# Optimization experiments

Measured on AMD Instinct MI355X. Metric: run time of the kernel, lower is better.

## Reference

```python
import jax, jax.numpy as jnp
import numpy as np

K_SIZE, STRIDE, PAD = 3, 1, 1
B, C1, C2, H, W = 2, 256, 256, 64, 64


def conv2d(x, w, b, stride, pad):
    out = jax.lax.conv_general_dilated(
        x, w, (stride, stride), [(pad, pad), (pad, pad)],
        dimension_numbers=("NCHW", "OIHW", "NCHW"))
    return out + b[None, :, None, None]


def deform_conv2d(x, offset, mask, w, b, k, stride, pad):
    # torchvision.ops.deform_conv2d semantics (modulated, offset_groups=1)
    Bn, C, Hh, Ww = x.shape
    Ho, Wo = offset.shape[2], offset.shape[3]
    K = k * k
    # offset channels are (dy, dx) interleaved per kernel point
    off = offset.reshape(Bn, K, 2, Ho, Wo)
    dy, dx = off[:, :, 0], off[:, :, 1]          # [B,K,Ho,Wo]
    ki = jnp.arange(k)
    kyy, kxx = jnp.meshgrid(ki, ki, indexing="ij")
    kyy, kxx = kyy.reshape(K), kxx.reshape(K)
    base_y = (jnp.arange(Ho) * stride - pad)[None, :, None] + kyy[:, None, None]  # [K,Ho,1]
    base_x = (jnp.arange(Wo) * stride - pad)[None, None, :] + kxx[:, None, None]  # [K,1,Wo]
    ys = base_y[None].astype(x.dtype) + dy       # [B,K,Ho,Wo]
    xs = base_x[None].astype(x.dtype) + dx
    N = K * Ho * Wo
    ysf, xsf = ys.reshape(Bn, N), xs.reshape(Bn, N)
    y0 = jnp.floor(ysf)
    x0 = jnp.floor(xsf)
    ly, lx = ysf - y0, xsf - x0                  # bilinear fractions
    y0i, x0i = y0.astype(jnp.int32), x0.astype(jnp.int32)
    xf = x.reshape(Bn, C, Hh * Ww)

    def gather(yi, xi):
        valid = (yi >= 0) & (yi < Hh) & (xi >= 0) & (xi < Ww)
        idx = jnp.clip(yi, 0, Hh - 1) * Ww + jnp.clip(xi, 0, Ww - 1)
        v = jnp.take_along_axis(xf, idx[:, None, :], axis=2)  # [B,C,N]
        return v * valid[:, None, :].astype(x.dtype)

    v00 = gather(y0i, x0i)
    v01 = gather(y0i, x0i + 1)
    v10 = gather(y0i + 1, x0i)
    v11 = gather(y0i + 1, x0i + 1)
    wy1, wx1 = ly[:, None], lx[:, None]
    val = (v00 * (1 - wy1) * (1 - wx1) + v01 * (1 - wy1) * wx1 +
           v10 * wy1 * (1 - wx1) + v11 * wy1 * wx1)          # [B,C,N]
    val = val.reshape(Bn, C, K, Ho, Wo) * mask[:, None]       # modulate
    out = jnp.einsum("ock,bckhw->bohw", w.reshape(w.shape[0], C, K), val)
    return out + b[None, :, None, None]


def setup_inputs() -> dict:
    key = jax.random.key(0)
    ks = jax.random.split(key, 6)
    k2 = K_SIZE * K_SIZE
    return {
        "x": jax.random.normal(ks[0], (B, C1, H, W), jnp.float32),
        "offset_feat": jax.random.normal(ks[1], (B, C2, H, W), jnp.float32),
        # offset/mask head conv (zero-init in module; small random so offsets are non-trivial)
        "w_offset_mask": jax.random.normal(ks[2], (3 * k2, C2, K_SIZE, K_SIZE), jnp.float32) * 0.01,
        "b_offset_mask": jax.random.normal(ks[3], (3 * k2,), jnp.float32) * 0.01,
        "w_dcn": jax.random.normal(ks[4], (C2, C1, K_SIZE, K_SIZE), jnp.float32) / np.sqrt(C1 * k2),
        "b_dcn": jax.random.normal(ks[5], (C2,), jnp.float32) * 0.01,
    }


def reference(x, offset_feat, w_offset_mask, b_offset_mask, w_dcn, b_dcn):
    om = conv2d(offset_feat, w_offset_mask, b_offset_mask, STRIDE, PAD)  # [B,3*k*k,Ho,Wo]
    o1, o2, m = jnp.split(om, 3, axis=1)
    offset = jnp.concatenate([o1, o2], axis=1)   # [B,2*k*k,Ho,Wo]
    mask = jax.nn.sigmoid(m)                      # [B,k*k,Ho,Wo]
    return deform_conv2d(x, offset, mask, w_dcn, b_dcn, K_SIZE, STRIDE, PAD)
```

## Files before the change

### kernel.cpp

```cpp
#include <hip/hip_runtime.h>
#include <math.h>

#define BATCH 2
#define CIN   256
#define COUT  256
#define COFF  256
#define HWPIX 4096
#define CKTOT 2304
#define VSTR  40
#define PH    66
#define PHW   4356
#define NKG   12

typedef __attribute__((ext_vector_type(8))) short short8;
typedef __attribute__((ext_vector_type(8))) unsigned short ushort8;
typedef __attribute__((ext_vector_type(4))) float float4v;

__device__ __forceinline__ unsigned short f2bf(float f) {
    unsigned u = __float_as_uint(f);
    unsigned r = (u + 0x7FFFu + ((u >> 16) & 1u)) >> 16;
    return (unsigned short)r;
}
__device__ __forceinline__ float bf2f(unsigned short h) {
    return __uint_as_float(((unsigned)h) << 16);
}

__global__ __launch_bounds__(256) void prep_kernel(
    const float* __restrict__ x, const float* __restrict__ feat,
    const float* __restrict__ wdcn, const float* __restrict__ wom,
    unsigned short* __restrict__ xTh,
    unsigned short* __restrict__ fh,
    unsigned short* __restrict__ whi,
    unsigned short* __restrict__ wohi,
    float* __restrict__ out)
{
    const int bid = blockIdx.x;
    const int tid = threadIdx.x;

    if (bid < 4096) {
        const bool isx = bid < 2048;
        const int lb = isx ? bid : bid - 2048;
        const int b  = lb >> 10;
        const int r  = lb & 1023;
        const int pt = r >> 3;
        const int ct = r & 7;
        __shared__ float t[32][33];
        const int tx = tid & 31, ty = tid >> 5;
        const float* src = isx ? x : feat;
        const float* sb = src + ((size_t)b * 256 + ct * 32) * HWPIX + pt * 32;
#pragma unroll
        for (int i = ty; i < 32; i += 8)
            t[i][tx] = sb[(size_t)i * HWPIX + tx];
        __syncthreads();
        if (isx) {
            unsigned short* ob = xTh + ((size_t)b * HWPIX + pt * 32) * 256 + ct * 32;
#pragma unroll
            for (int i = ty; i < 32; i += 8)
                ob[(size_t)i * 256 + tx] = f2bf(t[tx][i]);
        } else {
#pragma unroll
            for (int i = ty; i < 32; i += 8) {
                int p = pt * 32 + i;
                int row = (p >> 6) + 1, col = (p & 63) + 1;
                fh[((size_t)b * PHW + row * PH + col) * 256 + ct * 32 + tx]
                    = f2bf(t[tx][i]);
            }
        }
    } else if (bid < 6400) {
        int gid = (bid - 4096) * 256 + tid;
        int cc  = gid & 31;
        int co  = (gid >> 5) & 255;
        int kcb = gid >> 13;
        int k   = kcb >> 3;
        int cb  = kcb & 7;
        float w = wdcn[((size_t)co * 256 + cb * 32 + cc) * 9 + k];
        whi[gid] = f2bf(w);
    } else if (bid < 6688) {
        int gid = (bid - 6400) * 256 + tid;
        int cc  = gid & 31;
        int co  = (gid >> 5) & 31;
        int kcb = gid >> 10;
        int k   = kcb >> 3;
        int cb  = kcb & 7;
        float w = 0.0f;
        if (co < 27) w = wom[(size_t)co * CKTOT + (cb * 32 + cc) * 9 + k];
        wohi[gid] = f2bf(w);
    } else if (bid < 7208) {
        int idx = (bid - 6688) * 256 + tid;
        int b = idx / 66560;
        int r = idx - b * 66560;
        int pidx = r >> 8;
        int c = r & 255;
        int row, col;
        if (pidx < 66)       { row = 0;           col = pidx; }
        else if (pidx < 132) { row = 65;          col = pidx - 66; }
        else if (pidx < 196) { row = pidx - 131;  col = 0; }
        else                 { row = pidx - 195;  col = 65; }
        fh[((size_t)b * PHW + row * PH + col) * 256 + c] = 0;
    } else {
        int idx = (bid - 7208) * 256 + tid;
        ((float4*)out)[idx] = make_float4(0.f, 0.f, 0.f, 0.f);
    }
}

__global__ __launch_bounds__(256) void conv_om_mfma_kernel(
    const unsigned short* __restrict__ fh,
    const unsigned short* __restrict__ wohi,
    float* __restrict__ om12)
{
    const int y  = blockIdx.x;
    const int kg = blockIdx.y;
    const int b  = blockIdx.z;
    const int tid = threadIdx.x;
    const int wv  = tid >> 6;
    const int lane = tid & 63;
    const int l15 = lane & 15;
    const int q   = lane >> 4;
    const int xg  = wv * 16 + l15;

    float4v acc[2];
    acc[0] = (float4v)0.0f;
    acc[1] = (float4v)0.0f;

    const unsigned short* fhb = fh + (size_t)b * PHW * 256;

#pragma unroll 3
    for (int i = 0; i < 6; ++i) {
        int kcb = kg * 6 + i;
        int k  = kcb >> 3;
        int cb = kcb & 7;
        size_t s = ((size_t)((y + k / 3) * PH + xg + k % 3)) * 256 + cb * 32 + q * 8;
        short8 bh = *(const short8*)(fhb + s);
        short8 ah0 = *(const short8*)(wohi + ((size_t)kcb * 32 + l15) * 32 + q * 8);
        short8 ah1 = *(const short8*)(wohi + ((size_t)kcb * 32 + 16 + l15) * 32 + q * 8);
        acc[0] = __builtin_amdgcn_mfma_f32_16x16x32_bf16(ah0, bh, acc[0], 0, 0, 0);
        acc[1] = __builtin_amdgcn_mfma_f32_16x16x32_bf16(ah1, bh, acc[1], 0, 0, 0);
    }

    const int p = y * 64 + xg;
    float* ob = om12 + (size_t)(kg * 2 + b) * 27 * HWPIX;
#pragma unroll
    for (int t = 0; t < 2; ++t) {
#pragma unroll
        for (int r = 0; r < 4; ++r) {
            int co = t * 16 + q * 4 + r;
            if (co < 27) ob[co * HWPIX + p] = acc[t][r];
        }
    }
}

__global__ __launch_bounds__(256) void finalize_om_kernel(
    const float* __restrict__ om12,
    const float* __restrict__ bom,
    float4* __restrict__ wt4,
    int4*   __restrict__ ix4)
{
    const int gid = blockIdx.x * 256 + threadIdx.x;
    const int p  = gid & 4095;
    const int bk = gid >> 12;
    const int b  = bk / 9;
    const int k  = bk - b * 9;

    float dy = bom[2 * k], dx = bom[2 * k + 1], mm = bom[18 + k];
#pragma unroll
    for (int g = 0; g < NKG; ++g) {
        const float* ob = om12 + (size_t)(g * 2 + b) * 27 * HWPIX;
        dy += ob[(2 * k) * HWPIX + p];
        dx += ob[(2 * k + 1) * HWPIX + p];
        mm += ob[(18 + k) * HWPIX + p];
    }
    const int yy = p >> 6, xx = p & 63;
    float ys = (float)(yy - 1 + (k / 3)) + dy;
    float xs = (float)(xx - 1 + (k % 3)) + dx;
    float y0f = floorf(ys), x0f = floorf(xs);
    int y0 = (int)y0f, x0 = (int)x0f;
    float ly = ys - y0f, lx = xs - x0f;
    float m  = 1.0f / (1.0f + expf(-mm));
    bool yv0 = ((unsigned)y0 < 64u), yv1 = ((unsigned)(y0 + 1) < 64u);
    bool xv0 = ((unsigned)x0 < 64u), xv1 = ((unsigned)(x0 + 1) < 64u);
    int i00 = (y0 * 64 + x0) << 8;
    float4 wt;
    int4 ix;
    wt.x = (yv0 && xv0) ? (1.0f - ly) * (1.0f - lx) * m : 0.0f;
    wt.y = (yv0 && xv1) ? (1.0f - ly) * lx * m          : 0.0f;
    wt.z = (yv1 && xv0) ? ly * (1.0f - lx) * m          : 0.0f;
    wt.w = (yv1 && xv1) ? ly * lx * m                   : 0.0f;
    ix.x = (yv0 && xv0) ? i00          : 0;
    ix.y = (yv0 && xv1) ? i00 + 256    : 0;
    ix.z = (yv1 && xv0) ? i00 + 16384  : 0;
    ix.w = (yv1 && xv1) ? i00 + 16640  : 0;
    wt4[gid] = wt;
    ix4[gid] = ix;
}

__global__ __launch_bounds__(512, 4) void dcn_mfma_kernel(
    const unsigned short* __restrict__ xTh,
    const float4* __restrict__ wt4,
    const int4* __restrict__ ix4,
    const unsigned short* __restrict__ whi,
    const float* __restrict__ bdcn,
    float* __restrict__ out)
{
    const int tid = threadIdx.x;
    const int y   = blockIdx.x >> 1;
    const int xh  = blockIdx.x & 1;
    const int kg  = blockIdx.y;
    const int b   = blockIdx.z;

    __shared__ float4 s_wt[288];
    __shared__ int4   s_ix[288];
    __shared__ unsigned short V[288 * VSTR];

    if (tid < 288) {
        int k   = tid >> 5;
        int pxl = tid & 31;
        int p   = y * 64 + xh * 32 + pxl;
        int src = ((b * 9 + k) << 12) + p;
        s_wt[tid] = wt4[src];
        s_ix[tid] = ix4[src];
    }
    __syncthreads();

    const int w    = tid >> 6;
    const int lane = tid & 63;
    const int l15  = lane & 15;
    const int q    = lane >> 4;

    const int cg   = tid & 3;
    const int spx  = (tid >> 2) & 31;
    const int tapg = tid >> 7;

    float4v acc[2][2];
#pragma unroll
    for (int t = 0; t < 2; ++t)
#pragma unroll
        for (int p = 0; p < 2; ++p) acc[t][p] = (float4v)0.0f;

    const unsigned short* xb = xTh + ((size_t)b << 12) * 256;

    for (int cbl = 0; cbl < 4; ++cbl) {
        const int cb = kg * 4 + cbl;

        {
            const unsigned short* xc = xb + cb * 32 + cg * 8;
#pragma unroll 3
            for (int j = 0; j < 3; ++j) {
                int k = tapg + 4 * j;
                if (k > 8) break;
                int cidx = k * 32 + spx;
                float4 wt = s_wt[cidx];
                int4   ix = s_ix[cidx];
                ushort8 u00 = *(const ushort8*)(xc + ix.x);
                ushort8 u01 = *(const ushort8*)(xc + ix.y);
                ushort8 u10 = *(const ushort8*)(xc + ix.z);
                ushort8 u11 = *(const ushort8*)(xc + ix.w);
                unsigned hv[4];
#pragma unroll
                for (int jj = 0; jj < 4; ++jj) {
                    float va = wt.x * bf2f(u00[2 * jj])     + wt.y * bf2f(u01[2 * jj])
                             + wt.z * bf2f(u10[2 * jj])     + wt.w * bf2f(u11[2 * jj]);
                    float vb = wt.x * bf2f(u00[2 * jj + 1]) + wt.y * bf2f(u01[2 * jj + 1])
                             + wt.z * bf2f(u10[2 * jj + 1]) + wt.w * bf2f(u11[2 * jj + 1]);
                    hv[jj] = (unsigned)f2bf(va) | ((unsigned)f2bf(vb) << 16);
                }
                *(uint4*)&V[cidx * VSTR + cg * 8]
                    = make_uint4(hv[0], hv[1], hv[2], hv[3]);
            }
        }
        __syncthreads();

#pragma unroll 3
        for (int k = 0; k < 9; ++k) {
            const int kcb = k * 8 + cb;
            size_t base = ((size_t)kcb * 256 + w * 32 + l15) * 32 + q * 8;
            short8 ah0 = *(const short8*)(whi + base);
            short8 ah1 = *(const short8*)(whi + base + 16 * 32);
            short8 bh0 = *(const short8*)&V[(k * 32 + l15) * VSTR + q * 8];
            short8 bh1 = *(const short8*)&V[(k * 32 + 16 + l15) * VSTR + q * 8];
            acc[0][0] = __builtin_amdgcn_mfma_f32_16x16x32_bf16(ah0, bh0, acc[0][0], 0, 0, 0);
            acc[0][1] = __builtin_amdgcn_mfma_f32_16x16x32_bf16(ah0, bh1, acc[0][1], 0, 0, 0);
            acc[1][0] = __builtin_amdgcn_mfma_f32_16x16x32_bf16(ah1, bh0, acc[1][0], 0, 0, 0);
            acc[1][1] = __builtin_amdgcn_mfma_f32_16x16x32_bf16(ah1, bh1, acc[1][1], 0, 0, 0);
        }
        __syncthreads();
    }

#pragma unroll
    for (int t = 0; t < 2; ++t) {
#pragma unroll
        for (int r = 0; r < 4; ++r) {
            int co = w * 32 + t * 16 + q * 4 + r;
            float bias = (kg == 0) ? bdcn[co] : 0.0f;
#pragma unroll
            for (int p = 0; p < 2; ++p) {
                int px = xh * 32 + p * 16 + l15;
                atomicAdd(&out[(((size_t)b * COUT + co) << 12) + y * 64 + px],
                          acc[t][p][r] + bias);
            }
        }
    }
}

extern "C" void kernel_launch(void* const* d_in, const int* in_sizes, int n_in,
                              void* d_out, int out_size, void* d_ws, size_t ws_size,
                              hipStream_t stream)
{
    const float* x    = (const float*)d_in[0];
    const float* feat = (const float*)d_in[1];
    const float* wom  = (const float*)d_in[2];
    const float* bom  = (const float*)d_in[3];
    const float* wdcn = (const float*)d_in[4];
    const float* bdcn = (const float*)d_in[5];
    float* out = (float*)d_out;

    float* om12          = (float*)d_ws;
    unsigned short* whi  = (unsigned short*)(om12 + (size_t)NKG * 2 * 27 * HWPIX);
    unsigned short* wohi = whi + (size_t)CKTOT * 256;
    unsigned short* xTh  = wohi + 73728;
    unsigned short* fh   = xTh + (size_t)2 * HWPIX * 256;
    float4* wt4          = (float4*)(fh + (size_t)2 * PHW * 256);
    int4*   ix4          = (int4*)(wt4 + (size_t)2 * 9 * HWPIX);

    prep_kernel<<<9256, 256, 0, stream>>>(x, feat, wdcn, wom, xTh, fh,
                                          whi, wohi, out);

    dim3 gco(64, NKG, 2);
    conv_om_mfma_kernel<<<gco, 256, 0, stream>>>(fh, wohi, om12);

    finalize_om_kernel<<<288, 256, 0, stream>>>(om12, bom, wt4, ix4);

    dim3 grid(128, 2, 2);
    dcn_mfma_kernel<<<grid, 512, 0, stream>>>(xTh, wt4, ix4, whi, bdcn, out);
}
```

Measured before the change: 131.4 us.

## Fuse offset/mask conv with finalize via in-block split-K reduction in shared memory

The offset/mask conv previously split the 72 K-chunks across 12 block groups, wrote partial sums to a global om12 buffer, and a separate finalize kernel summed them and built the bilinear weights and indices. Now each block covers 16 pixels, each of its 4 waves handles 18 K-chunks, and the partials are reduced in shared memory. The same block then computes the sampling weights and indices directly. This removes one kernel launch and the global partial-sum round trip. In exchange there are fewer blocks (512 versus 1536), each with a longer serial MFMA chain, and only 144 of 256 threads do the finalize work.

```diff
diff --git a/kernel.cpp b/kernel.cpp
--- a/kernel.cpp
+++ b/kernel.cpp
@@ -10,7 +10,6 @@
 #define VSTR  40
 #define PH    66
 #define PHW   4356
-#define NKG   12
 
 typedef __attribute__((ext_vector_type(8))) short short8;
 typedef __attribute__((ext_vector_type(8))) unsigned short ushort8;
@@ -103,20 +102,24 @@
     }
 }
 
-__global__ __launch_bounds__(256) void conv_om_mfma_kernel(
+__global__ __launch_bounds__(256) void conv_om_fused_kernel(
     const unsigned short* __restrict__ fh,
     const unsigned short* __restrict__ wohi,
-    float* __restrict__ om12)
+    const float* __restrict__ bom,
+    float4* __restrict__ wt4,
+    int4*   __restrict__ ix4)
 {
-    const int y  = blockIdx.x;
-    const int kg = blockIdx.y;
-    const int b  = blockIdx.z;
-    const int tid = threadIdx.x;
-    const int wv  = tid >> 6;
+    const int tile = blockIdx.x;
+    const int b    = blockIdx.y;
+    const int y    = tile >> 2;
+    const int xb   = (tile & 3) * 16;
+    const int tid  = threadIdx.x;
+    const int wv   = tid >> 6;
     const int lane = tid & 63;
-    const int l15 = lane & 15;
-    const int q   = lane >> 4;
-    const int xg  = wv * 16 + l15;
+    const int l15  = lane & 15;
+    const int q    = lane >> 4;
+
+    __shared__ float red[4][32][16];
 
     float4v acc[2];
     acc[0] = (float4v)0.0f;
@@ -124,73 +127,59 @@
 
     const unsigned short* fhb = fh + (size_t)b * PHW * 256;
 
-#pragma unroll 3
-    for (int i = 0; i < 6; ++i) {
-        int kcb = kg * 6 + i;
+#pragma unroll 6
+    for (int i = 0; i < 18; ++i) {
+        int kcb = wv * 18 + i;
         int k  = kcb >> 3;
         int cb = kcb & 7;
-        size_t s = ((size_t)((y + k / 3) * PH + xg + k % 3)) * 256 + cb * 32 + q * 8;
-        short8 bh = *(const short8*)(fhb + s);
+        size_t s = ((size_t)((y + k / 3) * PH + xb + l15 + k % 3)) * 256 + cb * 32 + q * 8;
+        short8 bh  = *(const short8*)(fhb + s);
         short8 ah0 = *(const short8*)(wohi + ((size_t)kcb * 32 + l15) * 32 + q * 8);
         short8 ah1 = *(const short8*)(wohi + ((size_t)kcb * 32 + 16 + l15) * 32 + q * 8);
         acc[0] = __builtin_amdgcn_mfma_f32_16x16x32_bf16(ah0, bh, acc[0], 0, 0, 0);
         acc[1] = __builtin_amdgcn_mfma_f32_16x16x32_bf16(ah1, bh, acc[1], 0, 0, 0);
     }
 
-    const int p = y * 64 + xg;
-    float* ob = om12 + (size_t)(kg * 2 + b) * 27 * HWPIX;
-#pragma unroll
-    for (int t = 0; t < 2; ++t) {
-#pragma unroll
-        for (int r = 0; r < 4; ++r) {
-            int co = t * 16 + q * 4 + r;
-            if (co < 27) ob[co * HWPIX + p] = acc[t][r];
-        }
-    }
-}
-
-__global__ __launch_bounds__(256) void finalize_om_kernel(
-    const float* __restrict__ om12,
-    const float* __restrict__ bom,
-    float4* __restrict__ wt4,
-    int4*   __restrict__ ix4)
-{
-    const int gid = blockIdx.x * 256 + threadIdx.x;
-    const int p  = gid & 4095;
-    const int bk = gid >> 12;
-    const int b  = bk / 9;
-    const int k  = bk - b * 9;
-
-    float dy = bom[2 * k], dx = bom[2 * k + 1], mm = bom[18 + k];
-#pragma unroll
-    for (int g = 0; g < NKG; ++g) {
-        const float* ob = om12 + (size_t)(g * 2 + b) * 27 * HWPIX;
-        dy += ob[(2 * k) * HWPIX + p];
-        dx += ob[(2 * k + 1) * HWPIX + p];
-        mm += ob[(18 + k) * HWPIX + p];
-    }
-    const int yy = p >> 6, xx = p & 63;
-    float ys = (float)(yy - 1 + (k / 3)) + dy;
-    float xs = (float)(xx - 1 + (k % 3)) + dx;
-    float y0f = floorf(ys), x0f = floorf(xs);
-    int y0 = (int)y0f, x0 = (int)x0f;
-    float ly = ys - y0f, lx = xs - x0f;
-    float m  = 1.0f / (1.0f + expf(-mm));
-    bool yv0 = ((unsigned)y0 < 64u), yv1 = ((unsigned)(y0 + 1) < 64u);
-    bool xv0 = ((unsigned)x0 < 64u), xv1 = ((unsigned)(x0 + 1) < 64u);
-    int i00 = (y0 * 64 + x0) << 8;
-    float4 wt;
-    int4 ix;
-    wt.x = (yv0 && xv0) ? (1.0f - ly) * (1.0f - lx) * m : 0.0f;
-    wt.y = (yv0 && xv1) ? (1.0f - ly) * lx * m          : 0.0f;
-    wt.z = (yv1 && xv0) ? ly * (1.0f - lx) * m          : 0.0f;
-    wt.w = (yv1 && xv1) ? ly * lx * m                   : 0.0f;
-    ix.x = (yv0 && xv0) ? i00          : 0;
-    ix.y = (yv0 && xv1) ? i00 + 256    : 0;
-    ix.z = (yv1 && xv0) ? i00 + 16384  : 0;
-    ix.w = (yv1 && xv1) ? i00 + 16640  : 0;
-    wt4[gid] = wt;
-    ix4[gid] = ix;
+#pragma unroll
+    for (int t = 0; t < 2; ++t)
+#pragma unroll
+        for (int r = 0; r < 4; ++r)
+            red[wv][t * 16 + q * 4 + r][l15] = acc[t][r];
+    __syncthreads();
+
+    if (tid < 144) {
+        int k   = tid >> 4;
+        int pxl = tid & 15;
+        float dy = bom[2 * k]     + red[0][2 * k][pxl]     + red[1][2 * k][pxl]
+                                  + red[2][2 * k][pxl]     + red[3][2 * k][pxl];
+        float dx = bom[2 * k + 1] + red[0][2 * k + 1][pxl] + red[1][2 * k + 1][pxl]
+                                  + red[2][2 * k + 1][pxl] + red[3][2 * k + 1][pxl];
+        float mm = bom[18 + k]    + red[0][18 + k][pxl]    + red[1][18 + k][pxl]
+                                  + red[2][18 + k][pxl]    + red[3][18 + k][pxl];
+        int xx = xb + pxl;
+        float ys = (float)(y  - 1 + (k / 3)) + dy;
+        float xs = (float)(xx - 1 + (k % 3)) + dx;
+        float y0f = floorf(ys), x0f = floorf(xs);
+        int y0 = (int)y0f, x0 = (int)x0f;
+        float ly = ys - y0f, lx = xs - x0f;
+        float m  = 1.0f / (1.0f + expf(-mm));
+        bool yv0 = ((unsigned)y0 < 64u), yv1 = ((unsigned)(y0 + 1) < 64u);
+        bool xv0 = ((unsigned)x0 < 64u), xv1 = ((unsigned)(x0 + 1) < 64u);
+        int i00 = (y0 * 64 + x0) << 8;
+        float4 wt;
+        int4 ix;
+        wt.x = (yv0 && xv0) ? (1.0f - ly) * (1.0f - lx) * m : 0.0f;
+        wt.y = (yv0 && xv1) ? (1.0f - ly) * lx * m          : 0.0f;
+        wt.z = (yv1 && xv0) ? ly * (1.0f - lx) * m          : 0.0f;
+        wt.w = (yv1 && xv1) ? ly * lx * m                   : 0.0f;
+        ix.x = (yv0 && xv0) ? i00          : 0;
+        ix.y = (yv0 && xv1) ? i00 + 256    : 0;
+        ix.z = (yv1 && xv0) ? i00 + 16384  : 0;
+        ix.w = (yv1 && xv1) ? i00 + 16640  : 0;
+        int dst = ((b * 9 + k) << 12) + y * 64 + xx;
+        wt4[dst] = wt;
+        ix4[dst] = ix;
+    }
 }
 
 __global__ __launch_bounds__(512, 4) void dcn_mfma_kernel(
@@ -313,8 +302,7 @@
     const float* bdcn = (const float*)d_in[5];
     float* out = (float*)d_out;
 
-    float* om12          = (float*)d_ws;
-    unsigned short* whi  = (unsigned short*)(om12 + (size_t)NKG * 2 * 27 * HWPIX);
+    unsigned short* whi  = (unsigned short*)d_ws;
     unsigned short* wohi = whi + (size_t)CKTOT * 256;
     unsigned short* xTh  = wohi + 73728;
     unsigned short* fh   = xTh + (size_t)2 * HWPIX * 256;
@@ -324,10 +312,8 @@
     prep_kernel<<<9256, 256, 0, stream>>>(x, feat, wdcn, wom, xTh, fh,
                                           whi, wohi, out);
 
-    dim3 gco(64, NKG, 2);
-    conv_om_mfma_kernel<<<gco, 256, 0, stream>>>(fh, wohi, om12);
-
-    finalize_om_kernel<<<288, 256, 0, stream>>>(om12, bom, wt4, ix4);
+    dim3 gom(256, 2);
+    conv_om_fused_kernel<<<gom, 256, 0, stream>>>(fh, wohi, bom, wt4, ix4);
 
     dim3 grid(128, 2, 2);
     dcn_mfma_kernel<<<grid, 512, 0, stream>>>(xTh, wt4, ix4, whi, bdcn, out);
```

Measured after the change: 127.7 us. 2.8% less time.
